# Kernel optimization log

Hardware: AMD Instinct MI355X
Metric: run time of the kernel (lower is better)

The kernel has to match this reference:

```python
import math
import jax, jax.numpy as jnp
import numpy as np

DIM = 4096
N_HEADS = 32
N_KV_HEADS = 8
HEAD_DIM = DIM // N_HEADS  # 128
N_REP = N_HEADS // N_KV_HEADS  # 4
BSZ = 2
SEQLEN = 2048
ROPE_THETA = 500000.0


def setup_inputs() -> dict:
    key = jax.random.key(0)
    ks = jax.random.split(key, 6)
    s = 0.02
    x = jax.random.normal(ks[0], (BSZ, SEQLEN, DIM), dtype=jnp.float32)
    wq = jax.random.normal(ks[1], (DIM, N_HEADS * HEAD_DIM), dtype=jnp.float32) * s
    wk = jax.random.normal(ks[2], (DIM, N_KV_HEADS * HEAD_DIM), dtype=jnp.float32) * s
    wv = jax.random.normal(ks[3], (DIM, N_KV_HEADS * HEAD_DIM), dtype=jnp.float32) * s
    wo = jax.random.normal(ks[4], (N_HEADS * HEAD_DIM, DIM), dtype=jnp.float32) * s
    # RoPE frequencies (real cos/sin form of complex freqs_cis)
    inv_freq = 1.0 / (ROPE_THETA ** (jnp.arange(0, HEAD_DIM, 2, dtype=jnp.float32) / HEAD_DIM))
    t = jnp.arange(SEQLEN, dtype=jnp.float32)
    angles = jnp.outer(t, inv_freq)  # [S, HEAD_DIM/2]
    freqs_cos = jnp.cos(angles)
    freqs_sin = jnp.sin(angles)
    # additive causal mask [S, S]: 0 on/below diag, -1e9 above
    mask = jnp.where(jnp.tril(jnp.ones((SEQLEN, SEQLEN), dtype=bool)), 0.0, -1e9).astype(jnp.float32)
    return {"x": x, "wq": wq, "wk": wk, "wv": wv, "wo": wo,
            "freqs_cos": freqs_cos, "freqs_sin": freqs_sin, "mask": mask,
            "start_pos": 0}


def _apply_rope(t, cos, sin):
    # t: [B, S, H, HD]; cos/sin: [S, HD/2] -> broadcast [1, S, 1, HD/2]
    b, s, h, hd = t.shape
    tr = t.reshape(b, s, h, hd // 2, 2)
    te, to = tr[..., 0], tr[..., 1]
    c = cos[None, :, None, :]
    sn = sin[None, :, None, :]
    oe = te * c - to * sn
    oo = te * sn + to * c
    return jnp.stack([oe, oo], axis=-1).reshape(b, s, h, hd)


def reference(x, wq, wk, wv, wo, freqs_cos, freqs_sin, mask, start_pos):
    bsz, seqlen, _ = x.shape
    xq = (x @ wq).reshape(bsz, seqlen, N_HEADS, HEAD_DIM)
    xk = (x @ wk).reshape(bsz, seqlen, N_KV_HEADS, HEAD_DIM)
    xv = (x @ wv).reshape(bsz, seqlen, N_KV_HEADS, HEAD_DIM)
    xq = _apply_rope(xq, freqs_cos, freqs_sin)
    xk = _apply_rope(xk, freqs_cos, freqs_sin)
    # prefill: cache[:start_pos+seqlen] == xk/xv (start_pos=0); GQA repeat
    keys = jnp.repeat(xk, N_REP, axis=2)    # [B, S, N_HEADS, HD]
    values = jnp.repeat(xv, N_REP, axis=2)
    q = xq.transpose(0, 2, 1, 3)            # [B, H, S, HD]
    k = keys.transpose(0, 2, 1, 3)
    v = values.transpose(0, 2, 1, 3)
    scores = jnp.einsum('bhqd,bhkd->bhqk', q, k) / math.sqrt(HEAD_DIM)
    scores = scores + mask[None, None, :, :]
    probs = jax.nn.softmax(scores.astype(jnp.float32), axis=-1).astype(q.dtype)
    ctx = jnp.einsum('bhqk,bhkd->bhqd', probs, v)
    out = ctx.transpose(0, 2, 1, 3).reshape(bsz, seqlen, N_HEADS * HEAD_DIM)
    return out @ wo
```

## Files before the change

### kernel.cpp

```cpp
#include <hip/hip_runtime.h>
#include <hip/hip_bf16.h>
#include <math.h>
#include <stdint.h>

#define DIM 4096
#define N_HEADS 32
#define N_KV_HEADS 8
#define HEAD_DIM 128
#define BSZ 2
#define SEQLEN 2048
#define BS (BSZ * SEQLEN)
#define KV_DIM (N_KV_HEADS * HEAD_DIM)

typedef unsigned short u16;
typedef __attribute__((ext_vector_type(8))) short bf16x8;
typedef __attribute__((ext_vector_type(4))) float f32x4;
typedef __attribute__((ext_vector_type(8))) unsigned short u16x8;
typedef __attribute__((ext_vector_type(4))) unsigned short u16x4;

__device__ __forceinline__ u16 f2bf(float f) {
    __hip_bfloat16 h = __float2bfloat16(f);
    return *reinterpret_cast<u16*>(&h);
}
__device__ __forceinline__ float bf2f(u16 u) {
    __hip_bfloat16 h;
    *reinterpret_cast<u16*>(&h) = u;
    return __bfloat162float(h);
}

#define GLOAD_LDS16(gptr, lptr)                                                      \
    __builtin_amdgcn_global_load_lds(                                                \
        reinterpret_cast<const __attribute__((address_space(1))) uint32_t*>(         \
            reinterpret_cast<uintptr_t>(gptr)),                                      \
        reinterpret_cast<__attribute__((address_space(3))) uint32_t*>(               \
            reinterpret_cast<uintptr_t>(lptr)),                                      \
        16, 0, 0)

__global__ void cvt_f32_bf16(const float* __restrict__ in, u16* __restrict__ out, int n4) {
    int i = blockIdx.x * blockDim.x + threadIdx.x;
    if (i >= n4) return;
    float4 v = reinterpret_cast<const float4*>(in)[i];
    u16x4 o;
    o.x = f2bf(v.x); o.y = f2bf(v.y); o.z = f2bf(v.z); o.w = f2bf(v.w);
    reinterpret_cast<u16x4*>(out)[i] = o;
}

__global__ __launch_bounds__(256) void transpose_f32_bf16(const float* __restrict__ in,
                                                          u16* __restrict__ out,
                                                          int K, int N) {
    __shared__ float tile[32][33];
    const int tx = threadIdx.x, ty = threadIdx.y;
    const int n0 = blockIdx.x * 32, k0 = blockIdx.y * 32;
#pragma unroll
    for (int i = 0; i < 4; ++i)
        tile[ty + 8 * i][tx] = in[(size_t)(k0 + ty + 8 * i) * N + n0 + tx];
    __syncthreads();
#pragma unroll
    for (int i = 0; i < 4; ++i)
        out[(size_t)(n0 + ty + 8 * i) * K + k0 + tx] = f2bf(tile[tx][ty + 8 * i]);
}

__global__ __launch_bounds__(256) void transpose_v_bf16(const u16* __restrict__ xv,
                                                        u16* __restrict__ xvT) {
    __shared__ u16 tile[32][33];
    const int tx = threadIdx.x, ty = threadIdx.y;
    const int k0 = blockIdx.x * 32, d0 = blockIdx.y * 32;
    const int bh = blockIdx.z;
    const int b = bh >> 3, hkv = bh & 7;
#pragma unroll
    for (int i = 0; i < 4; ++i)
        tile[ty + 8 * i][tx] =
            xv[((size_t)(b * SEQLEN) + k0 + ty + 8 * i) * KV_DIM + hkv * HEAD_DIM + d0 + tx];
    __syncthreads();
#pragma unroll
    for (int i = 0; i < 4; ++i)
        xvT[((size_t)bh * HEAD_DIM + d0 + ty + 8 * i) * SEQLEN + k0 + tx] = tile[tx][ty + 8 * i];
}

template <bool OUT_BF16>
__global__ __launch_bounds__(256) void gemm_mfma_bt(const u16* __restrict__ A,
                                                    const u16* __restrict__ BT,
                                                    void* __restrict__ Cv,
                                                    int M, int N, int K) {
    __shared__ __align__(16) u16 Al[128 * 64];
    __shared__ __align__(16) u16 Bl[128 * 64];

    const int tid  = threadIdx.x;
    const int wave = tid >> 6;
    const int lane = tid & 63;
    const int quad = lane >> 4;
    const int lm   = lane & 15;
    const size_t bm = (size_t)blockIdx.y * 128;
    const size_t bn = (size_t)blockIdx.x * 128;
    const int wm = (wave & 1) * 64;
    const int wn = (wave >> 1) * 64;

    const int slot = lane & 7;
    const int lrow = lane >> 3;
    const int csw  = slot ^ (lrow & 7);

    f32x4 acc[4][4] = {};

    for (int k0 = 0; k0 < K; k0 += 64) {
        __syncthreads();
#pragma unroll
        for (int i = 0; i < 4; ++i) {
            const int mloc = wave * 32 + i * 8 + lrow;
            const u16* gA = A  + (bm + mloc) * (size_t)K + k0 + csw * 8;
            const u16* gB = BT + (bn + mloc) * (size_t)K + k0 + csw * 8;
            u16* lA = &Al[(mloc * 8 + slot) * 8];
            u16* lB = &Bl[(mloc * 8 + slot) * 8];
            GLOAD_LDS16(gA, lA);
            GLOAD_LDS16(gB, lB);
        }
        __syncthreads();

#pragma unroll
        for (int ks8 = 0; ks8 < 8; ks8 += 4) {
            bf16x8 af[4], bfr[4];
            const int cc = ks8 + quad;
#pragma unroll
            for (int i = 0; i < 4; ++i) {
                const int m = wm + 16 * i + lm;
                af[i]  = *(const bf16x8*)&Al[(m * 8 + (cc ^ (m & 7))) * 8];
                const int n = wn + 16 * i + lm;
                bfr[i] = *(const bf16x8*)&Bl[(n * 8 + (cc ^ (n & 7))) * 8];
            }
#pragma unroll
            for (int i = 0; i < 4; ++i)
#pragma unroll
                for (int j = 0; j < 4; ++j)
                    acc[i][j] = __builtin_amdgcn_mfma_f32_16x16x32_bf16(af[i], bfr[j], acc[i][j], 0, 0, 0);
        }
    }

#pragma unroll
    for (int i = 0; i < 4; ++i) {
        const int mrow = wm + 16 * i + quad * 4;
#pragma unroll
        for (int j = 0; j < 4; ++j) {
            const int ncol = wn + 16 * j + lm;
#pragma unroll
            for (int r = 0; r < 4; ++r) {
                const size_t off = (bm + mrow + r) * (size_t)N + bn + ncol;
                const float v = acc[i][j][r];
                if constexpr (OUT_BF16) ((u16*)Cv)[off] = f2bf(v);
                else                    ((float*)Cv)[off] = v;
            }
        }
    }
}

__global__ void rope_kernel(u16* __restrict__ t,
                            const float* __restrict__ cosb,
                            const float* __restrict__ sinb,
                            int n_heads, int total_pairs) {
    int idx = blockIdx.x * blockDim.x + threadIdx.x;
    if (idx >= total_pairs) return;
    int p = idx & 63;
    int h = (idx >> 6) % n_heads;
    int bs = idx / (64 * n_heads);
    int s = bs & (SEQLEN - 1);

    float c = cosb[s * 64 + p];
    float sn = sinb[s * 64 + p];

    size_t base = (size_t)bs * (n_heads * HEAD_DIM) + h * HEAD_DIM + 2 * p;
    float e = bf2f(t[base]);
    float o = bf2f(t[base + 1]);
    t[base]     = f2bf(e * c - o * sn);
    t[base + 1] = f2bf(e * sn + o * c);
}

__global__ __launch_bounds__(256) void flash_attn_mfma(const u16* __restrict__ xq,
                                                       const u16* __restrict__ xk,
                                                       const u16* __restrict__ xvT,
                                                       u16* __restrict__ ctx) {
    __shared__ __align__(16) u16 Ks[2][64 * 16 * 8];
    __shared__ __align__(16) u16 Vt[2][128 * 8 * 8];
    __shared__ __align__(16) u16 Ps[4][16 * 8 * 8];

    const int qt  = (int)gridDim.x - 1 - (int)blockIdx.x;
    const int h   = blockIdx.y;
    const int b   = blockIdx.z;
    const int hkv = h >> 2;

    const int tid  = threadIdx.x;
    const int wave = tid >> 6;
    const int lane = tid & 63;
    const int quad = lane >> 4;
    const int lm   = lane & 15;
    const int q0   = qt * 64;
    const float C = 0.08838834764831845f * 1.44269504088896f;

    const int ciK_r[4] = { (0 * 256 + tid) >> 4, (1 * 256 + tid) >> 4,
                           (2 * 256 + tid) >> 4, (3 * 256 + tid) >> 4 };

    bf16x8 qf[4];
    {
        const u16* qp = xq + ((size_t)(b * SEQLEN) + q0 + wave * 16 + lm) * DIM
                        + h * HEAD_DIM + quad * 8;
#pragma unroll
        for (int s = 0; s < 4; ++s) qf[s] = *(const bf16x8*)(qp + s * 32);
    }

    const u16* xkb = xk + (size_t)(b * SEQLEN) * KV_DIM + hkv * HEAD_DIM;
    const u16* xvb = xvT + ((size_t)(b * N_KV_HEADS + hkv)) * HEAD_DIM * SEQLEN;

    auto STAGE = [&](int kt, int sel) {
        const int k0 = kt * 64;
#pragma unroll
        for (int i = 0; i < 4; ++i) {
            const int ci = i * 256 + tid;
            const int kr = ci >> 4, cp = ci & 15;
            const u16* gK = xkb + (size_t)(k0 + kr) * KV_DIM + (cp ^ (kr & 7)) * 8;
            GLOAD_LDS16(gK, &Ks[sel][ci * 8]);
            const int dr = ci >> 3, cq = ci & 7;
            const u16* gV = xvb + (size_t)dr * SEQLEN + k0 + (cq ^ (dr & 7)) * 8;
            GLOAD_LDS16(gV, &Vt[sel][ci * 8]);
        }
    };

    float m_i[4], l_i[4];
#pragma unroll
    for (int r = 0; r < 4; ++r) { m_i[r] = -INFINITY; l_i[r] = 0.f; }
    f32x4 acc_o[8] = {};

    STAGE(0, 0);
    __syncthreads();

    for (int kt = 0; kt <= qt; ++kt) {
        const int sel = kt & 1;
        const int k0 = kt * 64;
        if (kt < qt) STAGE(kt + 1, sel ^ 1);

        const u16* ksb = &Ks[sel][0];
        const u16* vtb = &Vt[sel][0];
        f32x4 sacc[4] = {};
        __builtin_amdgcn_s_setprio(1);
#pragma unroll
        for (int ks = 0; ks < 4; ++ks) {
#pragma unroll
            for (int ct = 0; ct < 4; ++ct) {
                const int krow = ct * 16 + lm;
                bf16x8 kf = *(const bf16x8*)&ksb[(krow * 16 + ((ks * 4 + quad) ^ (krow & 7))) * 8];
                sacc[ct] = __builtin_amdgcn_mfma_f32_16x16x32_bf16(qf[ks], kf, sacc[ct], 0, 0, 0);
            }
        }
        __builtin_amdgcn_s_setprio(0);

        if (kt == qt) {
#pragma unroll
            for (int ct = 0; ct < 4; ++ct)
#pragma unroll
                for (int r = 0; r < 4; ++r)
                    if (k0 + ct * 16 + lm > q0 + wave * 16 + quad * 4 + r)
                        sacc[ct][r] = -1e30f;
        }

        float alpha[4];
#pragma unroll
        for (int r = 0; r < 4; ++r) {
            float mx = fmaxf(fmaxf(sacc[0][r], sacc[1][r]), fmaxf(sacc[2][r], sacc[3][r]));
#pragma unroll
            for (int off = 1; off < 16; off <<= 1) mx = fmaxf(mx, __shfl_xor(mx, off));
            const float nm = fmaxf(m_i[r], mx);
            alpha[r] = exp2f((m_i[r] - nm) * C);
            m_i[r] = nm;
            float sum = 0.f;
#pragma unroll
            for (int ct = 0; ct < 4; ++ct) {
                const float p = exp2f((sacc[ct][r] - nm) * C);
                sacc[ct][r] = p;
                sum += p;
            }
#pragma unroll
            for (int off = 1; off < 16; off <<= 1) sum += __shfl_xor(sum, off);
            l_i[r] = alpha[r] * l_i[r] + sum;
        }

        u16* ps = &Ps[wave][0];
#pragma unroll
        for (int ct = 0; ct < 4; ++ct)
#pragma unroll
            for (int r = 0; r < 4; ++r) {
                const int qq  = quad * 4 + r;
                const int col = ct * 16 + lm;
                ps[(qq * 8 + ((col >> 3) ^ (qq & 7))) * 8 + (col & 7)] = f2bf(sacc[ct][r]);
            }
        bf16x8 pf[2];
#pragma unroll
        for (int ks = 0; ks < 2; ++ks)
            pf[ks] = *(const bf16x8*)&ps[(lm * 8 + ((ks * 4 + quad) ^ (lm & 7))) * 8];

#pragma unroll
        for (int dt = 0; dt < 8; ++dt)
#pragma unroll
            for (int r = 0; r < 4; ++r) acc_o[dt][r] *= alpha[r];

        __builtin_amdgcn_s_setprio(1);
#pragma unroll
        for (int ks = 0; ks < 2; ++ks)
#pragma unroll
            for (int dt = 0; dt < 8; ++dt) {
                const int d = dt * 16 + lm;
                bf16x8 vf = *(const bf16x8*)&vtb[(d * 8 + ((ks * 4 + quad) ^ (d & 7))) * 8];
                acc_o[dt] = __builtin_amdgcn_mfma_f32_16x16x32_bf16(pf[ks], vf, acc_o[dt], 0, 0, 0);
            }
        __builtin_amdgcn_s_setprio(0);

        if (kt < qt) __syncthreads();
    }

    float inv_l[4];
#pragma unroll
    for (int r = 0; r < 4; ++r) inv_l[r] = 1.f / l_i[r];
    u16* op = ctx + ((size_t)(b * SEQLEN) + q0 + wave * 16 + quad * 4) * DIM + h * HEAD_DIM + lm;
#pragma unroll
    for (int r = 0; r < 4; ++r)
#pragma unroll
        for (int dt = 0; dt < 8; ++dt)
            op[(size_t)r * DIM + dt * 16] = f2bf(acc_o[dt][r] * inv_l[r]);
}

extern "C" void kernel_launch(void* const* d_in, const int* in_sizes, int n_in,
                              void* d_out, int out_size, void* d_ws, size_t ws_size,
                              hipStream_t stream) {
    const float* x   = (const float*)d_in[0];
    const float* wq  = (const float*)d_in[1];
    const float* wk  = (const float*)d_in[2];
    const float* wv  = (const float*)d_in[3];
    const float* wo  = (const float*)d_in[4];
    const float* fc  = (const float*)d_in[5];
    const float* fs  = (const float*)d_in[6];
    float* out = (float*)d_out;

    u16* x_bf = (u16*)d_ws;
    u16* wqT  = x_bf + (size_t)BS * DIM;
    u16* wkT  = wqT + (size_t)DIM * DIM;
    u16* wvT  = wkT + (size_t)KV_DIM * DIM;
    u16* woT  = wvT + (size_t)KV_DIM * DIM;
    u16* xq   = woT + (size_t)DIM * DIM;
    u16* xk   = xq + (size_t)BS * DIM;
    u16* xv   = xk + (size_t)BS * KV_DIM;
    u16* ctx  = x_bf;
    u16* xvT  = wvT;

    {
        int n4 = BS * DIM / 4;
        cvt_f32_bf16<<<(n4 + 255) / 256, 256, 0, stream>>>(x, x_bf, n4);
        dim3 blk(32, 8);
        transpose_f32_bf16<<<dim3(DIM / 32, DIM / 32), blk, 0, stream>>>(wq, wqT, DIM, DIM);
        transpose_f32_bf16<<<dim3(KV_DIM / 32, DIM / 32), blk, 0, stream>>>(wk, wkT, DIM, KV_DIM);
        transpose_f32_bf16<<<dim3(KV_DIM / 32, DIM / 32), blk, 0, stream>>>(wv, wvT, DIM, KV_DIM);
        transpose_f32_bf16<<<dim3(DIM / 32, DIM / 32), blk, 0, stream>>>(wo, woT, DIM, DIM);
    }

    gemm_mfma_bt<true><<<dim3(DIM / 128, BS / 128), 256, 0, stream>>>(x_bf, wqT, xq, BS, DIM, DIM);
    gemm_mfma_bt<true><<<dim3(KV_DIM / 128, BS / 128), 256, 0, stream>>>(x_bf, wkT, xk, BS, KV_DIM, DIM);
    gemm_mfma_bt<true><<<dim3(KV_DIM / 128, BS / 128), 256, 0, stream>>>(x_bf, wvT, xv, BS, KV_DIM, DIM);

    transpose_v_bf16<<<dim3(SEQLEN / 32, HEAD_DIM / 32, BSZ * N_KV_HEADS), dim3(32, 8), 0, stream>>>(xv, xvT);

    {
        int total_q = BS * N_HEADS * 64;
        rope_kernel<<<(total_q + 255) / 256, 256, 0, stream>>>(xq, fc, fs, N_HEADS, total_q);
        int total_k = BS * N_KV_HEADS * 64;
        rope_kernel<<<(total_k + 255) / 256, 256, 0, stream>>>(xk, fc, fs, N_KV_HEADS, total_k);
    }

    flash_attn_mfma<<<dim3(SEQLEN / 64, N_HEADS, BSZ), 256, 0, stream>>>(xq, xk, xvT, ctx);

    gemm_mfma_bt<false><<<dim3(DIM / 128, BS / 128), 256, 0, stream>>>(ctx, woT, out, BS, DIM, DIM);
}
```

Before: 1.133 ms.

## Rewrite flash attention with 32x32 MFMA, 128-row query tiles and register P

The attention kernel now processes 128 query rows per block, 32 per wave, using 32x32x16 MFMA with K/V as the A operand, so softmax statistics are per-lane. P is kept in registers via cross-half shuffles instead of a round trip through LDS. The output is staged through padded LDS for coalesced stores, and launch bounds request two blocks per CU. The K/V double buffering is removed in favour of a single buffer with two barriers per tile, which gives up load/compute overlap and adds more wasted masked work per block.

```diff
diff --git a/kernel.cpp b/kernel.cpp
--- a/kernel.cpp
+++ b/kernel.cpp
@@ -15,6 +15,7 @@
 typedef unsigned short u16;
 typedef __attribute__((ext_vector_type(8))) short bf16x8;
 typedef __attribute__((ext_vector_type(4))) float f32x4;
+typedef __attribute__((ext_vector_type(16))) float f32x16;
 typedef __attribute__((ext_vector_type(8))) unsigned short u16x8;
 typedef __attribute__((ext_vector_type(4))) unsigned short u16x4;
 
@@ -26,6 +27,9 @@
     __hip_bfloat16 h;
     *reinterpret_cast<u16*>(&h) = u;
     return __bfloat162float(h);
+}
+__device__ __forceinline__ uint32_t packbf(float a, float b) {
+    return (uint32_t)f2bf(a) | ((uint32_t)f2bf(b) << 16);
 }
 
 #define GLOAD_LDS16(gptr, lptr)                                                      \
@@ -172,13 +176,15 @@
     t[base + 1] = f2bf(e * sn + o * c);
 }
 
-__global__ __launch_bounds__(256) void flash_attn_mfma(const u16* __restrict__ xq,
-                                                       const u16* __restrict__ xk,
-                                                       const u16* __restrict__ xvT,
-                                                       u16* __restrict__ ctx) {
-    __shared__ __align__(16) u16 Ks[2][64 * 16 * 8];
-    __shared__ __align__(16) u16 Vt[2][128 * 8 * 8];
-    __shared__ __align__(16) u16 Ps[4][16 * 8 * 8];
+#define OPAD 132
+
+__global__ __launch_bounds__(256, 2) void flash_attn_mfma(const u16* __restrict__ xq,
+                                                          const u16* __restrict__ xk,
+                                                          const u16* __restrict__ xvT,
+                                                          u16* __restrict__ ctx) {
+    __shared__ __align__(16) u16 LB[128 * OPAD];
+    u16* Ks = LB;
+    u16* Vt = LB + 64 * 16 * 8;
 
     const int qt  = (int)gridDim.x - 1 - (int)blockIdx.x;
     const int h   = blockIdx.y;
@@ -188,139 +194,148 @@
     const int tid  = threadIdx.x;
     const int wave = tid >> 6;
     const int lane = tid & 63;
-    const int quad = lane >> 4;
-    const int lm   = lane & 15;
-    const int q0   = qt * 64;
+    const int hh   = lane >> 5;
+    const int l31  = lane & 31;
+    const int q0   = qt * 128;
+    const int wq0  = q0 + wave * 32;
+    const int qrow = wq0 + l31;
     const float C = 0.08838834764831845f * 1.44269504088896f;
 
-    const int ciK_r[4] = { (0 * 256 + tid) >> 4, (1 * 256 + tid) >> 4,
-                           (2 * 256 + tid) >> 4, (3 * 256 + tid) >> 4 };
-
-    bf16x8 qf[4];
+    bf16x8 qf[8];
     {
-        const u16* qp = xq + ((size_t)(b * SEQLEN) + q0 + wave * 16 + lm) * DIM
-                        + h * HEAD_DIM + quad * 8;
-#pragma unroll
-        for (int s = 0; s < 4; ++s) qf[s] = *(const bf16x8*)(qp + s * 32);
+        const u16* qp = xq + ((size_t)(b * SEQLEN) + qrow) * DIM + h * HEAD_DIM + hh * 8;
+#pragma unroll
+        for (int s = 0; s < 8; ++s) qf[s] = *(const bf16x8*)(qp + 16 * s);
     }
 
     const u16* xkb = xk + (size_t)(b * SEQLEN) * KV_DIM + hkv * HEAD_DIM;
     const u16* xvb = xvT + ((size_t)(b * N_KV_HEADS + hkv)) * HEAD_DIM * SEQLEN;
 
-    auto STAGE = [&](int kt, int sel) {
+    float m_i = -INFINITY, l_i = 0.f;
+    f32x16 acc[4] = {};
+
+    const int nkt = 2 * qt + 2;
+    for (int kt = 0; kt < nkt; ++kt) {
         const int k0 = kt * 64;
+        __syncthreads();
 #pragma unroll
         for (int i = 0; i < 4; ++i) {
             const int ci = i * 256 + tid;
             const int kr = ci >> 4, cp = ci & 15;
-            const u16* gK = xkb + (size_t)(k0 + kr) * KV_DIM + (cp ^ (kr & 7)) * 8;
-            GLOAD_LDS16(gK, &Ks[sel][ci * 8]);
+            GLOAD_LDS16(xkb + (size_t)(k0 + kr) * KV_DIM + (cp ^ (kr & 7)) * 8, &Ks[ci * 8]);
             const int dr = ci >> 3, cq = ci & 7;
-            const u16* gV = xvb + (size_t)dr * SEQLEN + k0 + (cq ^ (dr & 7)) * 8;
-            GLOAD_LDS16(gV, &Vt[sel][ci * 8]);
-        }
-    };
-
-    float m_i[4], l_i[4];
-#pragma unroll
-    for (int r = 0; r < 4; ++r) { m_i[r] = -INFINITY; l_i[r] = 0.f; }
-    f32x4 acc_o[8] = {};
-
-    STAGE(0, 0);
+            GLOAD_LDS16(xvb + (size_t)dr * SEQLEN + k0 + (cq ^ (dr & 7)) * 8, &Vt[ci * 8]);
+        }
+        __syncthreads();
+
+        if (k0 > wq0 + 31) continue;
+
+        f32x16 s[2] = {};
+        __builtin_amdgcn_s_setprio(1);
+#pragma unroll
+        for (int step = 0; step < 8; ++step) {
+#pragma unroll
+            for (int ct = 0; ct < 2; ++ct) {
+                const int krow = ct * 32 + l31;
+                const int c = 2 * step + hh;
+                bf16x8 kf = *(const bf16x8*)&Ks[(krow * 16 + (c ^ (krow & 7))) * 8];
+                s[ct] = __builtin_amdgcn_mfma_f32_32x32x16_bf16(kf, qf[step], s[ct], 0, 0, 0);
+            }
+        }
+        __builtin_amdgcn_s_setprio(0);
+
+        if (k0 + 63 > wq0) {
+#pragma unroll
+            for (int ct = 0; ct < 2; ++ct)
+#pragma unroll
+                for (int r = 0; r < 16; ++r) {
+                    const int kg = k0 + ct * 32 + (r & 3) + 8 * (r >> 2) + 4 * hh;
+                    if (kg > qrow) s[ct][r] = -1e30f;
+                }
+        }
+
+        float mx = s[0][0];
+#pragma unroll
+        for (int r = 1; r < 16; ++r) mx = fmaxf(mx, s[0][r]);
+#pragma unroll
+        for (int r = 0; r < 16; ++r) mx = fmaxf(mx, s[1][r]);
+        mx = fmaxf(mx, __shfl_xor(mx, 32));
+        const float nm = fmaxf(m_i, mx);
+        const float alpha = exp2f((m_i - nm) * C);
+        m_i = nm;
+        float sum = 0.f;
+#pragma unroll
+        for (int ct = 0; ct < 2; ++ct)
+#pragma unroll
+            for (int r = 0; r < 16; ++r) {
+                const float p = exp2f((s[ct][r] - nm) * C);
+                s[ct][r] = p;
+                sum += p;
+            }
+        sum += __shfl_xor(sum, 32);
+        l_i = alpha * l_i + sum;
+
+        bf16x8 pa[4];
+#pragma unroll
+        for (int ct = 0; ct < 2; ++ct)
+#pragma unroll
+            for (int kss = 0; kss < 2; ++kss) {
+                const int base = 8 * kss;
+                const uint32_t lo0 = packbf(s[ct][base + 0], s[ct][base + 1]);
+                const uint32_t lo1 = packbf(s[ct][base + 2], s[ct][base + 3]);
+                const uint32_t hi0 = packbf(s[ct][base + 4], s[ct][base + 5]);
+                const uint32_t hi1 = packbf(s[ct][base + 6], s[ct][base + 7]);
+                const uint32_t s0 = hh ? lo0 : hi0;
+                const uint32_t s1 = hh ? lo1 : hi1;
+                const uint32_t r0 = (uint32_t)__shfl_xor((int)s0, 32);
+                const uint32_t r1 = (uint32_t)__shfl_xor((int)s1, 32);
+                union { uint32_t u[4]; bf16x8 v; } pu;
+                pu.u[0] = hh ? r0 : lo0;
+                pu.u[1] = hh ? r1 : lo1;
+                pu.u[2] = hh ? hi0 : r0;
+                pu.u[3] = hh ? hi1 : r1;
+                pa[2 * ct + kss] = pu.v;
+            }
+
+#pragma unroll
+        for (int dt = 0; dt < 4; ++dt)
+#pragma unroll
+            for (int r = 0; r < 16; ++r) acc[dt][r] *= alpha;
+
+        __builtin_amdgcn_s_setprio(1);
+#pragma unroll
+        for (int ks = 0; ks < 4; ++ks)
+#pragma unroll
+            for (int dt = 0; dt < 4; ++dt) {
+                const int vrow = dt * 32 + l31;
+                const int c = 2 * ks + hh;
+                bf16x8 vf = *(const bf16x8*)&Vt[(vrow * 8 + (c ^ (vrow & 7))) * 8];
+                acc[dt] = __builtin_amdgcn_mfma_f32_32x32x16_bf16(vf, pa[ks], acc[dt], 0, 0, 0);
+            }
+        __builtin_amdgcn_s_setprio(0);
+    }
+
     __syncthreads();
-
-    for (int kt = 0; kt <= qt; ++kt) {
-        const int sel = kt & 1;
-        const int k0 = kt * 64;
-        if (kt < qt) STAGE(kt + 1, sel ^ 1);
-
-        const u16* ksb = &Ks[sel][0];
-        const u16* vtb = &Vt[sel][0];
-        f32x4 sacc[4] = {};
-        __builtin_amdgcn_s_setprio(1);
-#pragma unroll
-        for (int ks = 0; ks < 4; ++ks) {
-#pragma unroll
-            for (int ct = 0; ct < 4; ++ct) {
-                const int krow = ct * 16 + lm;
-                bf16x8 kf = *(const bf16x8*)&ksb[(krow * 16 + ((ks * 4 + quad) ^ (krow & 7))) * 8];
-                sacc[ct] = __builtin_amdgcn_mfma_f32_16x16x32_bf16(qf[ks], kf, sacc[ct], 0, 0, 0);
-            }
-        }
-        __builtin_amdgcn_s_setprio(0);
-
-        if (kt == qt) {
-#pragma unroll
-            for (int ct = 0; ct < 4; ++ct)
-#pragma unroll
-                for (int r = 0; r < 4; ++r)
-                    if (k0 + ct * 16 + lm > q0 + wave * 16 + quad * 4 + r)
-                        sacc[ct][r] = -1e30f;
-        }
-
-        float alpha[4];
-#pragma unroll
-        for (int r = 0; r < 4; ++r) {
-            float mx = fmaxf(fmaxf(sacc[0][r], sacc[1][r]), fmaxf(sacc[2][r], sacc[3][r]));
-#pragma unroll
-            for (int off = 1; off < 16; off <<= 1) mx = fmaxf(mx, __shfl_xor(mx, off));
-            const float nm = fmaxf(m_i[r], mx);
-            alpha[r] = exp2f((m_i[r] - nm) * C);
-            m_i[r] = nm;
-            float sum = 0.f;
-#pragma unroll
-            for (int ct = 0; ct < 4; ++ct) {
-                const float p = exp2f((sacc[ct][r] - nm) * C);
-                sacc[ct][r] = p;
-                sum += p;
-            }
-#pragma unroll
-            for (int off = 1; off < 16; off <<= 1) sum += __shfl_xor(sum, off);
-            l_i[r] = alpha[r] * l_i[r] + sum;
-        }
-
-        u16* ps = &Ps[wave][0];
-#pragma unroll
-        for (int ct = 0; ct < 4; ++ct)
-#pragma unroll
-            for (int r = 0; r < 4; ++r) {
-                const int qq  = quad * 4 + r;
-                const int col = ct * 16 + lm;
-                ps[(qq * 8 + ((col >> 3) ^ (qq & 7))) * 8 + (col & 7)] = f2bf(sacc[ct][r]);
-            }
-        bf16x8 pf[2];
-#pragma unroll
-        for (int ks = 0; ks < 2; ++ks)
-            pf[ks] = *(const bf16x8*)&ps[(lm * 8 + ((ks * 4 + quad) ^ (lm & 7))) * 8];
-
-#pragma unroll
-        for (int dt = 0; dt < 8; ++dt)
-#pragma unroll
-            for (int r = 0; r < 4; ++r) acc_o[dt][r] *= alpha[r];
-
-        __builtin_amdgcn_s_setprio(1);
-#pragma unroll
-        for (int ks = 0; ks < 2; ++ks)
-#pragma unroll
-            for (int dt = 0; dt < 8; ++dt) {
-                const int d = dt * 16 + lm;
-                bf16x8 vf = *(const bf16x8*)&vtb[(d * 8 + ((ks * 4 + quad) ^ (d & 7))) * 8];
-                acc_o[dt] = __builtin_amdgcn_mfma_f32_16x16x32_bf16(pf[ks], vf, acc_o[dt], 0, 0, 0);
-            }
-        __builtin_amdgcn_s_setprio(0);
-
-        if (kt < qt) __syncthreads();
-    }
-
-    float inv_l[4];
-#pragma unroll
-    for (int r = 0; r < 4; ++r) inv_l[r] = 1.f / l_i[r];
-    u16* op = ctx + ((size_t)(b * SEQLEN) + q0 + wave * 16 + quad * 4) * DIM + h * HEAD_DIM + lm;
-#pragma unroll
-    for (int r = 0; r < 4; ++r)
-#pragma unroll
-        for (int dt = 0; dt < 8; ++dt)
-            op[(size_t)r * DIM + dt * 16] = f2bf(acc_o[dt][r] * inv_l[r]);
+    const float inv_l = 1.0f / l_i;
+    const int q_l = wave * 32 + l31;
+#pragma unroll
+    for (int dt = 0; dt < 4; ++dt)
+#pragma unroll
+        for (int rp = 0; rp < 8; ++rp) {
+            const int reg = 2 * rp;
+            const int d = dt * 32 + (reg & 3) + 8 * (reg >> 2) + 4 * hh;
+            *(uint32_t*)&LB[q_l * OPAD + d] =
+                packbf(acc[dt][reg] * inv_l, acc[dt][reg + 1] * inv_l);
+        }
+    __syncthreads();
+    {
+        const int qr = tid >> 1, hf = tid & 1;
+        u16* op = ctx + ((size_t)(b * SEQLEN) + q0 + qr) * DIM + h * HEAD_DIM + hf * 64;
+        const u16* lp = &LB[qr * OPAD + hf * 64];
+#pragma unroll
+        for (int c = 0; c < 16; ++c)
+            *(u16x4*)(op + 4 * c) = *(const u16x4*)(lp + 4 * c);
+    }
 }
 
 extern "C" void kernel_launch(void* const* d_in, const int* in_sizes, int n_in,
@@ -369,7 +384,7 @@
         rope_kernel<<<(total_k + 255) / 256, 256, 0, stream>>>(xk, fc, fs, N_KV_HEADS, total_k);
     }
 
-    flash_attn_mfma<<<dim3(SEQLEN / 64, N_HEADS, BSZ), 256, 0, stream>>>(xq, xk, xvT, ctx);
+    flash_attn_mfma<<<dim3(SEQLEN / 128, N_HEADS, BSZ), 256, 0, stream>>>(xq, xk, xvT, ctx);
 
     gemm_mfma_bt<false><<<dim3(DIM / 128, BS / 128), 256, 0, stream>>>(ctx, woT, out, BS, DIM, DIM);
 }
```

Measured after the change: 993.6 us. 1.14x faster.
